# Kernel tuning notes

Measured on AMD Instinct MI355X. Metric: run time of the kernel, lower is better.

Reference implementation:

```python
import jax, jax.numpy as jnp
import numpy as np

N = 50000      # nodes
E = 400000     # edges per meta-path
DIN = 256      # input_dim
H = 4          # heads
F = 64         # output_dim per head
P = 3          # meta-paths
HID = 128      # SA_Attention hidden
NEG_SLOPE = 0.2


def setup_inputs() -> dict:
    key = jax.random.key(0)
    ks = jax.random.split(key, 12)
    inp = {
        "h": jax.random.normal(ks[0], (N, DIN), dtype=jnp.float32),
        "ei_0": jax.random.randint(ks[1], (2, E), 0, N, dtype=jnp.int64),
        "ei_1": jax.random.randint(ks[2], (2, E), 0, N, dtype=jnp.int64),
        "ei_2": jax.random.randint(ks[3], (2, E), 0, N, dtype=jnp.int64),
        # GAT params per meta-path (stacked over P)
        "gat_W": jax.random.normal(ks[4], (P, DIN, H * F), dtype=jnp.float32) * 0.05,
        "att_src": jax.random.normal(ks[5], (P, H, F), dtype=jnp.float32) * 0.05,
        "att_dst": jax.random.normal(ks[6], (P, H, F), dtype=jnp.float32) * 0.05,
        "gat_bias": jnp.zeros((P, H * F), dtype=jnp.float32),
        # SA_Attention params: Linear(H*F, HID) + Tanh + Linear(HID, 1, bias=False)
        "sa_w1": jax.random.normal(ks[7], (H * F, HID), dtype=jnp.float32) * 0.05,
        "sa_b1": jnp.zeros((HID,), dtype=jnp.float32),
        "sa_w2": jax.random.normal(ks[8], (HID,), dtype=jnp.float32) * 0.05,
    }
    return inp


def _gat_conv(x, ei, W, a_src, a_dst, b):
    """PyG-style GATConv with self-loops, concat heads. x:[N,DIN] -> [N,H*F]."""
    n = x.shape[0]
    xw = (x @ W).reshape(n, H, F)                    # [N,H,F]
    loop = jnp.arange(n, dtype=ei.dtype)
    src = jnp.concatenate([ei[0], loop])             # [E+N]
    dst = jnp.concatenate([ei[1], loop])
    alpha_s = jnp.einsum('nhf,hf->nh', xw, a_src)    # [N,H]
    alpha_d = jnp.einsum('nhf,hf->nh', xw, a_dst)
    e = jax.nn.leaky_relu(alpha_s[src] + alpha_d[dst], NEG_SLOPE)  # [E+N,H]
    # segment softmax over destination nodes (every node has a self loop)
    m = jax.ops.segment_max(e, dst, num_segments=n)
    ex = jnp.exp(e - m[dst])
    s = jax.ops.segment_sum(ex, dst, num_segments=n)
    alpha = ex / s[dst]                              # [E+N,H]
    out = jax.ops.segment_sum(alpha[:, :, None] * xw[src], dst, num_segments=n)
    return out.reshape(n, H * F) + b


def reference(h, ei_0, ei_1, ei_2, gat_W, att_src, att_dst, gat_bias,
              sa_w1, sa_b1, sa_w2):
    eis = [ei_0, ei_1, ei_2]
    # per-meta-path GAT embeddings -> z: [N, P, H*F]
    z = jnp.stack([
        _gat_conv(h, eis[i], gat_W[i], att_src[i], att_dst[i], gat_bias[i])
        for i in range(P)
    ], axis=1)
    # semantic attention: project -> mean over nodes -> softmax over meta-paths
    w = jnp.tanh(z @ sa_w1 + sa_b1) @ sa_w2          # [N,P]
    beta = jax.nn.softmax(w.mean(axis=0))            # [P]
    return (beta[None, :, None] * z).sum(axis=1)     # [N, H*F]
```

## Files before the change

### kernel.cpp

```cpp
#include <hip/hip_runtime.h>
#include <hip/hip_bf16.h>

__device__ __forceinline__ float bf2f(unsigned short u) {
    union { unsigned int i; float f; } x;
    x.i = ((unsigned int)u) << 16;
    return x.f;
}
__device__ __forceinline__ unsigned short f2bf(float f) {
    union { float f; unsigned int u; } x; x.f = f;
    unsigned int r = x.u + 0x7FFFu + ((x.u >> 16) & 1u);
    return (unsigned short)(r >> 16);
}
__device__ __forceinline__ float fast_tanh(float x) {
    float a = fabsf(x);
    float t = __expf(2.f * a);
    float r = 1.f - 2.f / (t + 1.f);
    return copysignf(r, x);
}

typedef __bf16    bf16x8 __attribute__((ext_vector_type(8)));
typedef _Float16  f16x8  __attribute__((ext_vector_type(8)));
typedef _Float16  f16x4  __attribute__((ext_vector_type(4)));
typedef float     f32x4  __attribute__((ext_vector_type(4)));
typedef unsigned short u16x8 __attribute__((ext_vector_type(8)));

#define XW_OFF     0UL
#define ZB_OFF     25600000UL
#define CSR_OFF    102400000UL
#define RS_OFF     107200000UL
#define CUR_OFF    107800064UL
#define BS_OFF     108400128UL
#define AS_OFF     108401152UL
#define AD_OFF     109201152UL
#define WT_OFF     110001152UL
#define W1T_OFF    110394368UL
#define ASF_OFF    110459904UL
#define ADF_OFF    110462976UL
#define BIASF_OFF  110466048UL
#define B1F_OFF    110469120UL
#define W2F_OFF    110469632UL
#define WSUM_OFF   110470144UL
#define BETA_OFF   110470208UL
#define FLAG_OFF   110470272UL

#define CHUNKA 5000
#define NBMAX  152
#define CAPB   16384

__global__ void probe(const unsigned short* __restrict__ hraw,
                      const unsigned int* __restrict__ eraw,
                      int* __restrict__ flags) {
    if (threadIdx.x == 0 && blockIdx.x == 0) {
        int sane = 0;
        for (int i = 0; i < 256; ++i) {
            unsigned int e = (hraw[i] >> 7) & 0xFF;
            if (hraw[i] != 0 && e >= 100 && e <= 150) sane++;
        }
        flags[0] = (sane >= 220) ? 1 : 0;
        int zeros = 0;
        for (int i = 1; i < 256; i += 2) if (eraw[i] == 0u) zeros++;
        flags[1] = (zeros >= 120) ? 1 : 0;
    }
}

__device__ __forceinline__ float rd_f(const void* p, int j, bool bf) {
    return bf ? bf2f(((const unsigned short*)p)[j]) : ((const float*)p)[j];
}
__device__ __forceinline__ int rd_i(const void* p, long long j, bool i64) {
    return i64 ? (int)((const long long*)p)[j] : ((const int*)p)[j];
}

__global__ void ingest_params(const void* W, const void* as, const void* ad, const void* bias,
                              const void* w1, const void* b1, const void* w2,
                              unsigned short* Wt, _Float16* w1t,
                              float* asf, float* adf, float* biasf,
                              float* b1f, float* w2f,
                              const int* __restrict__ flags) {
    int i = blockIdx.x * 256 + threadIdx.x;
    bool bf = flags[0] != 0;
    if (i < 196608) {
        int p = i >> 16, n = (i >> 8) & 255, k = i & 255;
        Wt[i] = f2bf(rd_f(W, p * 65536 + k * 256 + n, bf));
    } else if (i < 229376) {
        int j = i - 196608;
        int n = j >> 8, k = j & 255;
        w1t[j] = (_Float16)rd_f(w1, k * 128 + n, bf);
    } else if (i < 230144) {
        int j = i - 229376; asf[j] = rd_f(as, j, bf);
    } else if (i < 230912) {
        int j = i - 230144; adf[j] = rd_f(ad, j, bf);
    } else if (i < 231680) {
        int j = i - 230912; biasf[j] = rd_f(bias, j, bf);
    } else if (i < 231808) {
        int j = i - 231680; b1f[j] = rd_f(b1, j, bf);
    } else if (i < 231936) {
        int j = i - 231808; w2f[j] = rd_f(w2, j, bf);
    }
}

__global__ __launch_bounds__(256)
void bucket_a(const void* e0, const void* e1, const void* e2,
              int* __restrict__ bcnt, unsigned int* __restrict__ bkt,
              int E, int N, int NB, const int* __restrict__ flags) {
    __shared__ unsigned int  ent[CHUNKA];
    __shared__ unsigned char bck[CHUNKA];
    __shared__ unsigned int  sent[CHUNKA];
    __shared__ unsigned char sbck[CHUNKA];
    __shared__ int lcnt[NBMAX], lpre[NBMAX], lbase[NBMAX], lcur[NBMAX];
    int tid = threadIdx.x;
    int s = blockIdx.x * CHUNKA;
    int tot = 3 * E;
    int n = min(tot, s + CHUNKA) - s;
    for (int b = tid; b < NBMAX; b += 256) { lcnt[b] = 0; lcur[b] = 0; }
    __syncthreads();
    bool i64 = flags[1] != 0;
    for (int i = tid; i < n; i += 256) {
        int idx = s + i;
        int p = (idx >= 2 * E) ? 2 : (idx >= E) ? 1 : 0;
        int j = idx - p * E;
        const void* ep = (p == 0) ? e0 : (p == 1) ? e1 : e2;
        unsigned int src = (unsigned int)rd_i(ep, j, i64);
        unsigned int dst = (unsigned int)rd_i(ep, (long long)E + j, i64);
        int seg = p * N + (int)dst;
        int b = seg >> 10;
        ent[i] = src | ((unsigned int)(seg & 1023) << 16);
        bck[i] = (unsigned char)b;
        atomicAdd(&lcnt[b], 1);
    }
    __syncthreads();
    if (tid == 0) {
        int run = 0;
        for (int b = 0; b < NB; ++b) { lpre[b] = run; run += lcnt[b]; }
    }
    if (tid < NB) lbase[tid] = atomicAdd(&bcnt[tid], lcnt[tid]);
    __syncthreads();
    for (int i = tid; i < n; i += 256) {
        int b = bck[i];
        int pos = lpre[b] + atomicAdd(&lcur[b], 1);
        sent[pos] = ent[i];
        sbck[pos] = (unsigned char)b;
    }
    __syncthreads();
    for (int q = tid; q < n; q += 256) {
        int b = sbck[q];
        int gpos = lbase[b] + (q - lpre[b]);
        if (gpos < CAPB) bkt[(size_t)b * CAPB + gpos] = sent[q];
    }
}

__global__ __launch_bounds__(256)
void bucket_b(const int* __restrict__ bcnt, const unsigned int* __restrict__ bkt,
              int* __restrict__ rs, unsigned short* __restrict__ csr,
              int M, int NB, int tot) {
    __shared__ int scnt[1024];
    __shared__ int spre[1024];
    __shared__ int part[256];
    int b = blockIdx.x, tid = threadIdx.x;
    int acc = 0;
    for (int i = tid; i < b; i += 256) acc += min(bcnt[i], CAPB);
    part[tid] = acc; __syncthreads();
    for (int o = 128; o > 0; o >>= 1) {
        if (tid < o) part[tid] += part[tid + o];
        __syncthreads();
    }
    int base = part[0];
    int cnt = min(bcnt[b], CAPB);
    for (int i = tid; i < 1024; i += 256) scnt[i] = 0;
    __syncthreads();
    const unsigned int* src = bkt + (size_t)b * CAPB;
    for (int i = tid; i < cnt; i += 256)
        atomicAdd(&scnt[src[i] >> 16], 1);
    __syncthreads();
    int a0 = scnt[tid * 4], a1 = scnt[tid * 4 + 1], a2 = scnt[tid * 4 + 2], a3 = scnt[tid * 4 + 3];
    int psum = a0 + a1 + a2 + a3;
    part[tid] = psum; __syncthreads();
    for (int o = 1; o < 256; o <<= 1) {
        int tmp = (tid >= o) ? part[tid - o] : 0;
        __syncthreads();
        part[tid] += tmp;
        __syncthreads();
    }
    int pb = part[tid] - psum;
    spre[tid * 4]     = pb;
    spre[tid * 4 + 1] = pb + a0;
    spre[tid * 4 + 2] = pb + a0 + a1;
    spre[tid * 4 + 3] = pb + a0 + a1 + a2;
    __syncthreads();
    for (int i = tid; i < 1024; i += 256) {
        int seg = b * 1024 + i;
        if (seg < M) rs[seg] = base + spre[i];
        scnt[i] = 0;
    }
    if (b == NB - 1 && tid == 0) rs[M] = tot;
    __syncthreads();
    for (int i = tid; i < cnt; i += 256) {
        unsigned int u = src[i];
        int slow = u >> 16;
        int pos = spre[slow] + atomicAdd(&scnt[slow], 1);
        csr[base + pos] = (unsigned short)(u & 0xFFFFu);
    }
}

__global__ __launch_bounds__(1024, 4)
void gemm_xw_mfma(const void* __restrict__ h,
                  const unsigned short* __restrict__ Wtp,
                  unsigned short* __restrict__ xw,
                  const float* __restrict__ asf,
                  const float* __restrict__ adf,
                  float* __restrict__ as_, float* __restrict__ ad_,
                  const int* __restrict__ flags, int N) {
    __shared__ __bf16 Bs[32768];
    int tid  = threadIdx.x;
    int D = blockIdx.x;
    int qch = gridDim.x >> 3;
    int logical = (D & 7) * qch + (D >> 3);
    int ch   = logical & 1;
    int rg   = logical >> 1;
    {
        const bf16x8* src = (const bf16x8*)Wtp;
#pragma unroll
        for (int it = 0; it < 4; ++it) {
            int c = it * 1024 + tid;
            int row = c >> 5, cv = c & 31;
            *(bf16x8*)(Bs + ((row << 5) + (cv ^ (row & 7))) * 8) =
                src[(ch * 128 + row) * 32 + cv];
        }
    }
    __syncthreads();

    int wave = tid >> 6, lane = tid & 63;
    int l15 = lane & 15, quad = lane >> 4;
    int sw  = l15 & 7;
    int row0 = rg * 256 + wave * 16;
    bool bfm = flags[0] != 0;

    int lr = min(row0 + l15, N - 1);

    bf16x8 a[8];
    if (bfm) {
        const bf16x8* hp = reinterpret_cast<const bf16x8*>((const __bf16*)h + (size_t)lr * 256);
#pragma unroll
        for (int t = 0; t < 8; ++t) a[t] = hp[t * 4 + quad];
    } else {
        const float* hp = (const float*)h + (size_t)lr * 256;
#pragma unroll
        for (int t = 0; t < 8; ++t) {
            int off = t * 32 + quad * 8;
            f32x4 u0 = *reinterpret_cast<const f32x4*>(hp + off);
            f32x4 u1 = *reinterpret_cast<const f32x4*>(hp + off + 4);
#pragma unroll
            for (int j = 0; j < 4; ++j) { a[t][j] = (__bf16)u0[j]; a[t][4 + j] = (__bf16)u1[j]; }
        }
    }

    f32x4 acc[8];
#pragma unroll
    for (int tn = 0; tn < 8; ++tn) acc[tn] = (f32x4){0.f, 0.f, 0.f, 0.f};

#pragma unroll
    for (int t = 0; t < 8; ++t) {
        int c0 = t * 4;
#pragma unroll
        for (int tn = 0; tn < 8; ++tn) {
            int row = tn * 16 + l15;
            bf16x8 b = *reinterpret_cast<const bf16x8*>(
                Bs + ((row << 5) + ((c0 + quad) ^ sw)) * 8);
            acc[tn] = __builtin_amdgcn_mfma_f32_16x16x32_bf16(a[t], b, acc[tn], 0, 0, 0);
        }
    }

    int rbase = row0 + quad * 4;
#pragma unroll
    for (int tn = 0; tn < 8; ++tn) {
        int c = ch * 128 + tn * 16 + l15;
#pragma unroll
        for (int i = 0; i < 4; ++i) {
            int r = rbase + i;
            if (r < N) xw[(size_t)r * 256 + c] = f2bf(acc[tn][i]);
        }
    }
    float ss[2][4] = {{0.f,0.f,0.f,0.f},{0.f,0.f,0.f,0.f}};
    float dd[2][4] = {{0.f,0.f,0.f,0.f},{0.f,0.f,0.f,0.f}};
#pragma unroll
    for (int tn = 0; tn < 8; ++tn) {
        int c = ch * 128 + tn * 16 + l15;
        float sv = asf[c], dv = adf[c];
        int hs = tn >> 2;
#pragma unroll
        for (int i = 0; i < 4; ++i) {
            ss[hs][i] += acc[tn][i] * sv;
            dd[hs][i] += acc[tn][i] * dv;
        }
    }
#pragma unroll
    for (int hs = 0; hs < 2; ++hs)
#pragma unroll
        for (int i = 0; i < 4; ++i) {
            float s = ss[hs][i], d = dd[hs][i];
            s += __shfl_xor(s, 1); d += __shfl_xor(d, 1);
            s += __shfl_xor(s, 2); d += __shfl_xor(d, 2);
            s += __shfl_xor(s, 4); d += __shfl_xor(d, 4);
            s += __shfl_xor(s, 8); d += __shfl_xor(d, 8);
            ss[hs][i] = s; dd[hs][i] = d;
        }
    if (l15 == 0) {
#pragma unroll
        for (int hs = 0; hs < 2; ++hs)
#pragma unroll
            for (int i = 0; i < 4; ++i) {
                int r = rbase + i;
                if (r < N) {
                    int g = r * 4 + ch * 2 + hs;
                    as_[g] = ss[hs][i];
                    ad_[g] = dd[hs][i];
                }
            }
    }
}

__device__ __forceinline__ float leaky(float v) { return v > 0.f ? v : 0.2f * v; }

__global__ void agg_csr(const unsigned short* __restrict__ csr, const int* __restrict__ rs,
                        const float* __restrict__ as_, const float* __restrict__ ad_,
                        const unsigned short* __restrict__ xw,
                        const float* __restrict__ biasf,
                        _Float16* __restrict__ zb, int N, int p) {
    int d = blockIdx.x * 4 + (threadIdx.x >> 6);
    if (d >= N) return;
    int lane = threadIdx.x & 63;
    int half = lane >> 5;
    int l31  = lane & 31;
    int col8 = l31 * 8;
    int h    = col8 >> 6;
    int seg = p * N + d;
    int start = rs[seg], end = rs[seg + 1];

    float adh = ad_[d * 4 + h];
    float m = leaky(as_[d * 4 + h] + adh);
    float l = (half == 0) ? 1.f : 0.f;
    float a[8];
    {
        u16x8 u = *reinterpret_cast<const u16x8*>(xw + (size_t)d * 256 + col8);
#pragma unroll
        for (int k = 0; k < 8; ++k) a[k] = (half == 0) ? bf2f(u[k]) : 0.f;
    }

    if (start < end) {
        int i0 = min(start + half, end - 1);
        int srcA = csr[i0];
        float eA = (start + half < end) ? leaky(as_[srcA * 4 + h] + adh) : -1e30f;
        u16x8 xA = *reinterpret_cast<const u16x8*>(xw + (size_t)srcA * 256 + col8);
        for (int jb = start; jb < end; jb += 2) {
            int nidx = jb + 2 + half;
            int ni = min(nidx, end - 1);
            int srcB = csr[ni];
            float eB = (nidx < end) ? leaky(as_[srcB * 4 + h] + adh) : -1e30f;
            u16x8 xB = *reinterpret_cast<const u16x8*>(xw + (size_t)srcB * 256 + col8);
            float eO = __shfl_xor(eA, 32);
            float mn = fmaxf(m, fmaxf(eA, eO));
            float c  = __expf(m - mn);
            float w  = __expf(eA - mn);
            m = mn;
            l = l * c + w;
#pragma unroll
            for (int k = 0; k < 8; ++k)
                a[k] = a[k] * c + w * bf2f(xA[k]);
            srcA = srcB; eA = eB; xA = xB;
        }
    }
    l += __shfl_xor(l, 32);
#pragma unroll
    for (int k = 0; k < 8; ++k) a[k] += __shfl_xor(a[k], 32);

    if (half == 0) {
        float inv = 1.f / l;
        const float* bp = biasf + p * 256 + col8;
        f16x8 o;
#pragma unroll
        for (int k = 0; k < 8; ++k) o[k] = (_Float16)(a[k] * inv + bp[k]);
        *reinterpret_cast<f16x8*>(zb + ((size_t)d * 3 + p) * 256 + col8) = o;
    }
}

__global__ __launch_bounds__(1024, 4)
void sem_w_mfma(const _Float16* __restrict__ zb,
                const _Float16* __restrict__ w1t,
                const float* __restrict__ b1f,
                const float* __restrict__ w2f,
                float* __restrict__ wsum, int rows) {
    __shared__ _Float16 Bs[32768];
    __shared__ float redbuf[16][3];
    int tid = threadIdx.x;
    {
        const f16x8* src = (const f16x8*)w1t;
#pragma unroll
        for (int it = 0; it < 4; ++it) {
            int c = it * 1024 + tid;
            int row = c >> 5, cv = c & 31;
            *(f16x8*)(Bs + ((row << 5) + (cv ^ (row & 7))) * 8) = src[c];
        }
    }
    __syncthreads();

    int wave = tid >> 6, lane = tid & 63;
    int l15 = lane & 15, quad = lane >> 4;
    int sw  = l15 & 7;
    int row0 = blockIdx.x * 256 + wave * 16;
    int lr = min(row0 + l15, rows - 1);

    f16x8 a[8];
    {
        const f16x8* zp = reinterpret_cast<const f16x8*>(zb + (size_t)lr * 256);
#pragma unroll
        for (int t = 0; t < 8; ++t) a[t] = zp[t * 4 + quad];
    }

    f32x4 acc[8];
#pragma unroll
    for (int tn = 0; tn < 8; ++tn) acc[tn] = (f32x4){0.f, 0.f, 0.f, 0.f};

#pragma unroll
    for (int t = 0; t < 8; ++t) {
        int c0 = t * 4;
#pragma unroll
        for (int tn = 0; tn < 8; ++tn) {
            int brow = tn * 16 + l15;
            f16x8 b = *reinterpret_cast<const f16x8*>(
                Bs + ((brow << 5) + ((c0 + quad) ^ sw)) * 8);
            acc[tn] = __builtin_amdgcn_mfma_f32_16x16x32_f16(a[t], b, acc[tn], 0, 0, 0);
        }
    }

    float rowsum[4] = {0.f, 0.f, 0.f, 0.f};
#pragma unroll
    for (int tn = 0; tn < 8; ++tn) {
        int col = tn * 16 + l15;
        float b1v = b1f[col], w2v = w2f[col];
#pragma unroll
        for (int i = 0; i < 4; ++i)
            rowsum[i] += fast_tanh(acc[tn][i] + b1v) * w2v;
    }
#pragma unroll
    for (int i = 0; i < 4; ++i) {
        rowsum[i] += __shfl_xor(rowsum[i], 1);
        rowsum[i] += __shfl_xor(rowsum[i], 2);
        rowsum[i] += __shfl_xor(rowsum[i], 4);
        rowsum[i] += __shfl_xor(rowsum[i], 8);
    }
    float bins[3] = {0.f, 0.f, 0.f};
    if (l15 == 0) {
#pragma unroll
        for (int i = 0; i < 4; ++i) {
            int r = row0 + quad * 4 + i;
            if (r < rows) bins[r % 3] += rowsum[i];
        }
    }
#pragma unroll
    for (int b = 0; b < 3; ++b) {
        bins[b] += __shfl_xor(bins[b], 16);
        bins[b] += __shfl_xor(bins[b], 32);
    }
    if (lane == 0) {
#pragma unroll
        for (int b = 0; b < 3; ++b) redbuf[wave][b] = bins[b];
    }
    __syncthreads();
    if (tid < 3) {
        float s = 0.f;
#pragma unroll
        for (int w = 0; w < 16; ++w) s += redbuf[w][tid];
        atomicAdd(&wsum[tid], s);
    }
}

__global__ void combine(const _Float16* __restrict__ zb,
                        const float* __restrict__ wsum, float invN,
                        void* __restrict__ out, const int* __restrict__ flags) {
    int idx = blockIdx.x * 256 + threadIdx.x;
    int n = idx >> 6, c4 = (idx & 63) * 4;
    float w0 = wsum[0] * invN, w1 = wsum[1] * invN, w2 = wsum[2] * invN;
    float mx = fmaxf(w0, fmaxf(w1, w2));
    float e0 = __expf(w0 - mx), e1 = __expf(w1 - mx), e2 = __expf(w2 - mx);
    float s = 1.f / (e0 + e1 + e2);
    float b0 = e0 * s, b1 = e1 * s, b2 = e2 * s;
    const _Float16* base = zb + (size_t)n * 768 + c4;
    f16x4 z0 = *reinterpret_cast<const f16x4*>(base);
    f16x4 z1 = *reinterpret_cast<const f16x4*>(base + 256);
    f16x4 z2 = *reinterpret_cast<const f16x4*>(base + 512);
    float v[4];
#pragma unroll
    for (int i = 0; i < 4; ++i)
        v[i] = b0 * (float)z0[i] + b1 * (float)z1[i] + b2 * (float)z2[i];
    if (flags[0]) {
        ushort4 o = {f2bf(v[0]), f2bf(v[1]), f2bf(v[2]), f2bf(v[3])};
        *reinterpret_cast<ushort4*>((unsigned short*)out + (size_t)idx * 4) = o;
    } else {
        f32x4 o = {v[0], v[1], v[2], v[3]};
        *reinterpret_cast<f32x4*>((float*)out + (size_t)idx * 4) = o;
    }
}

extern "C" void kernel_launch(void* const* d_in, const int* in_sizes, int n_in,
                              void* d_out, int out_size, void* d_ws, size_t ws_size,
                              hipStream_t stream) {
    const void* h    = d_in[0];
    const void* e0   = d_in[1];
    const void* e1   = d_in[2];
    const void* e2   = d_in[3];
    const void* W    = d_in[4];
    const void* as   = d_in[5];
    const void* ad   = d_in[6];
    const void* bias = d_in[7];
    const void* w1   = d_in[8];
    const void* b1   = d_in[9];
    const void* w2   = d_in[10];

    const int N = in_sizes[0] / 256;
    const int E = in_sizes[1] / 2;
    const int M = 3 * N;
    const int NB = (M + 1023) >> 10;

    char* ws = (char*)d_ws;
    unsigned short* xw    = (unsigned short*)(ws + XW_OFF);
    _Float16*       zb    = (_Float16*)(ws + ZB_OFF);
    unsigned short* csr   = (unsigned short*)(ws + CSR_OFF);
    int*            rs    = (int*)(ws + RS_OFF);
    unsigned short* Wt    = (unsigned short*)(ws + WT_OFF);
    _Float16*       w1t   = (_Float16*)(ws + W1T_OFF);
    float*          asf   = (float*)(ws + ASF_OFF);
    float*          adf   = (float*)(ws + ADF_OFF);
    float*          biasf = (float*)(ws + BIASF_OFF);
    float*          b1f   = (float*)(ws + B1F_OFF);
    float*          w2f   = (float*)(ws + W2F_OFF);
    float*          wsum  = (float*)(ws + WSUM_OFF);
    float*          as_   = (float*)(ws + AS_OFF);
    float*          ad_   = (float*)(ws + AD_OFF);
    int*            flags = (int*)(ws + FLAG_OFF);

    unsigned int* bkt  = (unsigned int*)(ws + ZB_OFF);
    int*          bcnt = (int*)(ws + ZB_OFF + (size_t)NBMAX * CAPB * 4);

    probe<<<1, 64, 0, stream>>>((const unsigned short*)h, (const unsigned int*)e0, flags);
    ingest_params<<<907, 256, 0, stream>>>(W, as, ad, bias, w1, b1, w2,
                                           Wt, w1t, asf, adf, biasf, b1f, w2f, flags);

    hipMemsetAsync(bcnt, 0, NBMAX * sizeof(int), stream);
    int aBlocks = (3 * E + CHUNKA - 1) / CHUNKA;
    bucket_a<<<aBlocks, 256, 0, stream>>>(e0, e1, e2, bcnt, bkt, E, N, NB, flags);
    bucket_b<<<NB, 256, 0, stream>>>(bcnt, bkt, rs, csr, M, NB, 3 * E);

    hipMemsetAsync(wsum, 0, 16, stream);

    int gemmBlocks = ((N + 255) / 256) * 2;
    int aggBlocks  = (N + 3) / 4;
    for (int p = 0; p < 3; ++p) {
        gemm_xw_mfma<<<gemmBlocks, 1024, 0, stream>>>(h, Wt + p * 65536, xw,
                                                      asf + p * 256, adf + p * 256,
                                                      as_, ad_, flags, N);
        agg_csr<<<aggBlocks, 256, 0, stream>>>(csr, rs, as_, ad_, xw, biasf, zb, N, p);
    }

    int semBlocks = (M + 255) / 256;
    sem_w_mfma<<<semBlocks, 1024, 0, stream>>>(zb, w1t, b1f, w2f, wsum, M);
    combine<<<(N * 64 + 255) / 256, 256, 0, stream>>>(zb, wsum, 1.0f / (float)N, d_out, flags);
}
```

Measured before the change: 442.5 us.

## Fuse the three per-meta-path XW GEMMs into one launch reusing loaded h rows

The GEMM kernel now loops over all three meta-path weight matrices inside one launch. It loads each block's h row fragment into registers once and reloads only the weight tile into LDS per path. Separate xw and attention-score buffers are kept per path, and the workspace layout is recomputed so they fit, falling back to the old per-path launches if the workspace is too small. This cuts repeated reads of h and two launches, but costs about three times the xw buffer and gives up any overlap between GEMM and aggregation.

Result: no change. 449.0 us (+1.5%).

```diff
diff --git a/kernel.cpp b/kernel.cpp
--- a/kernel.cpp
+++ b/kernel.cpp
@@ -28,8 +28,6 @@
 #define ZB_OFF     25600000UL
 #define CSR_OFF    102400000UL
 #define RS_OFF     107200000UL
-#define CUR_OFF    107800064UL
-#define BS_OFF     108400128UL
 #define AS_OFF     108401152UL
 #define AD_OFF     109201152UL
 #define WT_OFF     110001152UL
@@ -40,7 +38,6 @@
 #define B1F_OFF    110469120UL
 #define W2F_OFF    110469632UL
 #define WSUM_OFF   110470144UL
-#define BETA_OFF   110470208UL
 #define FLAG_OFF   110470272UL
 
 #define CHUNKA 5000
@@ -203,12 +200,12 @@
 
 __global__ __launch_bounds__(1024, 4)
 void gemm_xw_mfma(const void* __restrict__ h,
-                  const unsigned short* __restrict__ Wtp,
+                  const unsigned short* __restrict__ Wt,
                   unsigned short* __restrict__ xw,
                   const float* __restrict__ asf,
                   const float* __restrict__ adf,
                   float* __restrict__ as_, float* __restrict__ ad_,
-                  const int* __restrict__ flags, int N) {
+                  const int* __restrict__ flags, int N, int pcount) {
     __shared__ __bf16 Bs[32768];
     int tid  = threadIdx.x;
     int D = blockIdx.x;
@@ -216,24 +213,12 @@
     int logical = (D & 7) * qch + (D >> 3);
     int ch   = logical & 1;
     int rg   = logical >> 1;
-    {
-        const bf16x8* src = (const bf16x8*)Wtp;
-#pragma unroll
-        for (int it = 0; it < 4; ++it) {
-            int c = it * 1024 + tid;
-            int row = c >> 5, cv = c & 31;
-            *(bf16x8*)(Bs + ((row << 5) + (cv ^ (row & 7))) * 8) =
-                src[(ch * 128 + row) * 32 + cv];
-        }
-    }
-    __syncthreads();
 
     int wave = tid >> 6, lane = tid & 63;
     int l15 = lane & 15, quad = lane >> 4;
     int sw  = l15 & 7;
     int row0 = rg * 256 + wave * 16;
     bool bfm = flags[0] != 0;
-
     int lr = min(row0 + l15, N - 1);
 
     bf16x8 a[8];
@@ -253,68 +238,88 @@
         }
     }
 
-    f32x4 acc[8];
-#pragma unroll
-    for (int tn = 0; tn < 8; ++tn) acc[tn] = (f32x4){0.f, 0.f, 0.f, 0.f};
-
-#pragma unroll
-    for (int t = 0; t < 8; ++t) {
-        int c0 = t * 4;
+    for (int p = 0; p < pcount; ++p) {
+        if (p) __syncthreads();
+        {
+            const bf16x8* src = (const bf16x8*)(Wt + (size_t)p * 65536);
+#pragma unroll
+            for (int it = 0; it < 4; ++it) {
+                int c = it * 1024 + tid;
+                int row = c >> 5, cv = c & 31;
+                *(bf16x8*)(Bs + ((row << 5) + (cv ^ (row & 7))) * 8) =
+                    src[(ch * 128 + row) * 32 + cv];
+            }
+        }
+        __syncthreads();
+
+        f32x4 acc[8];
+#pragma unroll
+        for (int tn = 0; tn < 8; ++tn) acc[tn] = (f32x4){0.f, 0.f, 0.f, 0.f};
+
+#pragma unroll
+        for (int t = 0; t < 8; ++t) {
+            int c0 = t * 4;
+#pragma unroll
+            for (int tn = 0; tn < 8; ++tn) {
+                int row = tn * 16 + l15;
+                bf16x8 b = *reinterpret_cast<const bf16x8*>(
+                    Bs + ((row << 5) + ((c0 + quad) ^ sw)) * 8);
+                acc[tn] = __builtin_amdgcn_mfma_f32_16x16x32_bf16(a[t], b, acc[tn], 0, 0, 0);
+            }
+        }
+
+        unsigned short* xwp = xw + (size_t)p * N * 256;
+        const float* asfp = asf + p * 256;
+        const float* adfp = adf + p * 256;
+        float* asp = as_ + (size_t)p * N * 4;
+        float* adp = ad_ + (size_t)p * N * 4;
+        int rbase = row0 + quad * 4;
 #pragma unroll
         for (int tn = 0; tn < 8; ++tn) {
-            int row = tn * 16 + l15;
-            bf16x8 b = *reinterpret_cast<const bf16x8*>(
-                Bs + ((row << 5) + ((c0 + quad) ^ sw)) * 8);
-            acc[tn] = __builtin_amdgcn_mfma_f32_16x16x32_bf16(a[t], b, acc[tn], 0, 0, 0);
-        }
-    }
-
-    int rbase = row0 + quad * 4;
-#pragma unroll
-    for (int tn = 0; tn < 8; ++tn) {
-        int c = ch * 128 + tn * 16 + l15;
-#pragma unroll
-        for (int i = 0; i < 4; ++i) {
-            int r = rbase + i;
-            if (r < N) xw[(size_t)r * 256 + c] = f2bf(acc[tn][i]);
-        }
-    }
-    float ss[2][4] = {{0.f,0.f,0.f,0.f},{0.f,0.f,0.f,0.f}};
-    float dd[2][4] = {{0.f,0.f,0.f,0.f},{0.f,0.f,0.f,0.f}};
-#pragma unroll
-    for (int tn = 0; tn < 8; ++tn) {
-        int c = ch * 128 + tn * 16 + l15;
-        float sv = asf[c], dv = adf[c];
-        int hs = tn >> 2;
-#pragma unroll
-        for (int i = 0; i < 4; ++i) {
-            ss[hs][i] += acc[tn][i] * sv;
-            dd[hs][i] += acc[tn][i] * dv;
-        }
-    }
-#pragma unroll
-    for (int hs = 0; hs < 2; ++hs)
-#pragma unroll
-        for (int i = 0; i < 4; ++i) {
-            float s = ss[hs][i], d = dd[hs][i];
-            s += __shfl_xor(s, 1); d += __shfl_xor(d, 1);
-            s += __shfl_xor(s, 2); d += __shfl_xor(d, 2);
-            s += __shfl_xor(s, 4); d += __shfl_xor(d, 4);
-            s += __shfl_xor(s, 8); d += __shfl_xor(d, 8);
-            ss[hs][i] = s; dd[hs][i] = d;
-        }
-    if (l15 == 0) {
-#pragma unroll
-        for (int hs = 0; hs < 2; ++hs)
+            int c = ch * 128 + tn * 16 + l15;
 #pragma unroll
             for (int i = 0; i < 4; ++i) {
                 int r = rbase + i;
-                if (r < N) {
-                    int g = r * 4 + ch * 2 + hs;
-                    as_[g] = ss[hs][i];
-                    ad_[g] = dd[hs][i];
+                if (r < N) xwp[(size_t)r * 256 + c] = f2bf(acc[tn][i]);
+            }
+        }
+        float ss[2][4] = {{0.f,0.f,0.f,0.f},{0.f,0.f,0.f,0.f}};
+        float dd[2][4] = {{0.f,0.f,0.f,0.f},{0.f,0.f,0.f,0.f}};
+#pragma unroll
+        for (int tn = 0; tn < 8; ++tn) {
+            int c = ch * 128 + tn * 16 + l15;
+            float sv = asfp[c], dv = adfp[c];
+            int hs = tn >> 2;
+#pragma unroll
+            for (int i = 0; i < 4; ++i) {
+                ss[hs][i] += acc[tn][i] * sv;
+                dd[hs][i] += acc[tn][i] * dv;
+            }
+        }
+#pragma unroll
+        for (int hs = 0; hs < 2; ++hs)
+#pragma unroll
+            for (int i = 0; i < 4; ++i) {
+                float s = ss[hs][i], d = dd[hs][i];
+                s += __shfl_xor(s, 1); d += __shfl_xor(d, 1);
+                s += __shfl_xor(s, 2); d += __shfl_xor(d, 2);
+                s += __shfl_xor(s, 4); d += __shfl_xor(d, 4);
+                s += __shfl_xor(s, 8); d += __shfl_xor(d, 8);
+                ss[hs][i] = s; dd[hs][i] = d;
+            }
+        if (l15 == 0) {
+#pragma unroll
+            for (int hs = 0; hs < 2; ++hs)
+#pragma unroll
+                for (int i = 0; i < 4; ++i) {
+                    int r = rbase + i;
+                    if (r < N) {
+                        int g = r * 4 + ch * 2 + hs;
+                        asp[g] = ss[hs][i];
+                        adp[g] = dd[hs][i];
+                    }
                 }
-            }
+        }
     }
 }
 
@@ -521,24 +526,66 @@
     const int NB = (M + 1023) >> 10;
 
     char* ws = (char*)d_ws;
-    unsigned short* xw    = (unsigned short*)(ws + XW_OFF);
-    _Float16*       zb    = (_Float16*)(ws + ZB_OFF);
-    unsigned short* csr   = (unsigned short*)(ws + CSR_OFF);
-    int*            rs    = (int*)(ws + RS_OFF);
-    unsigned short* Wt    = (unsigned short*)(ws + WT_OFF);
-    _Float16*       w1t   = (_Float16*)(ws + W1T_OFF);
-    float*          asf   = (float*)(ws + ASF_OFF);
-    float*          adf   = (float*)(ws + ADF_OFF);
-    float*          biasf = (float*)(ws + BIASF_OFF);
-    float*          b1f   = (float*)(ws + B1F_OFF);
-    float*          w2f   = (float*)(ws + W2F_OFF);
-    float*          wsum  = (float*)(ws + WSUM_OFF);
-    float*          as_   = (float*)(ws + AS_OFF);
-    float*          ad_   = (float*)(ws + AD_OFF);
-    int*            flags = (int*)(ws + FLAG_OFF);
-
-    unsigned int* bkt  = (unsigned int*)(ws + ZB_OFF);
-    int*          bcnt = (int*)(ws + ZB_OFF + (size_t)NBMAX * CAPB * 4);
+
+    auto al = [](size_t x) { return (x + 255) & ~(size_t)255; };
+    size_t o = 0;
+    size_t oXW3 = o; o += al((size_t)3 * N * 256 * 2);
+    size_t oZB  = o; o += al((size_t)3 * N * 256 * 2);
+    size_t oCSR = o; o += al((size_t)3 * E * 2);
+    size_t oRS  = o; o += al((size_t)(3 * N + 1) * 4);
+    size_t oAS3 = o; o += al((size_t)3 * N * 4 * 4);
+    size_t oAD3 = o; o += al((size_t)3 * N * 4 * 4);
+    size_t oWT  = o; o += al(196608UL * 2);
+    size_t oW1T = o; o += al(32768UL * 2);
+    size_t oASF = o; o += al(768 * 4);
+    size_t oADF = o; o += al(768 * 4);
+    size_t oBIA = o; o += al(768 * 4);
+    size_t oB1  = o; o += al(128 * 4);
+    size_t oW2  = o; o += al(128 * 4);
+    size_t oWSU = o; o += al(64);
+    size_t oFLG = o; o += al(64);
+    bool fused = (ws_size >= o);
+
+    unsigned short *xw, *csr, *Wt;
+    _Float16 *zb, *w1t;
+    int *rs, *flags;
+    float *asf, *adf, *biasf, *b1f, *w2f, *wsum, *as_, *ad_;
+    if (fused) {
+        xw    = (unsigned short*)(ws + oXW3);
+        zb    = (_Float16*)(ws + oZB);
+        csr   = (unsigned short*)(ws + oCSR);
+        rs    = (int*)(ws + oRS);
+        as_   = (float*)(ws + oAS3);
+        ad_   = (float*)(ws + oAD3);
+        Wt    = (unsigned short*)(ws + oWT);
+        w1t   = (_Float16*)(ws + oW1T);
+        asf   = (float*)(ws + oASF);
+        adf   = (float*)(ws + oADF);
+        biasf = (float*)(ws + oBIA);
+        b1f   = (float*)(ws + oB1);
+        w2f   = (float*)(ws + oW2);
+        wsum  = (float*)(ws + oWSU);
+        flags = (int*)(ws + oFLG);
+    } else {
+        xw    = (unsigned short*)(ws + XW_OFF);
+        zb    = (_Float16*)(ws + ZB_OFF);
+        csr   = (unsigned short*)(ws + CSR_OFF);
+        rs    = (int*)(ws + RS_OFF);
+        as_   = (float*)(ws + AS_OFF);
+        ad_   = (float*)(ws + AD_OFF);
+        Wt    = (unsigned short*)(ws + WT_OFF);
+        w1t   = (_Float16*)(ws + W1T_OFF);
+        asf   = (float*)(ws + ASF_OFF);
+        adf   = (float*)(ws + ADF_OFF);
+        biasf = (float*)(ws + BIASF_OFF);
+        b1f   = (float*)(ws + B1F_OFF);
+        w2f   = (float*)(ws + W2F_OFF);
+        wsum  = (float*)(ws + WSUM_OFF);
+        flags = (int*)(ws + FLAG_OFF);
+    }
+
+    unsigned int* bkt  = (unsigned int*)zb;
+    int*          bcnt = (int*)((char*)zb + (size_t)NBMAX * CAPB * 4);
 
     probe<<<1, 64, 0, stream>>>((const unsigned short*)h, (const unsigned int*)e0, flags);
     ingest_params<<<907, 256, 0, stream>>>(W, as, ad, bias, w1, b1, w2,
@@ -553,11 +600,22 @@
 
     int gemmBlocks = ((N + 255) / 256) * 2;
     int aggBlocks  = (N + 3) / 4;
-    for (int p = 0; p < 3; ++p) {
-        gemm_xw_mfma<<<gemmBlocks, 1024, 0, stream>>>(h, Wt + p * 65536, xw,
-                                                      asf + p * 256, adf + p * 256,
-                                                      as_, ad_, flags, N);
-        agg_csr<<<aggBlocks, 256, 0, stream>>>(csr, rs, as_, ad_, xw, biasf, zb, N, p);
+    if (fused) {
+        gemm_xw_mfma<<<gemmBlocks, 1024, 0, stream>>>(h, Wt, xw, asf, adf,
+                                                      as_, ad_, flags, N, 3);
+        for (int p = 0; p < 3; ++p)
+            agg_csr<<<aggBlocks, 256, 0, stream>>>(csr, rs,
+                                                   as_ + (size_t)p * N * 4,
+                                                   ad_ + (size_t)p * N * 4,
+                                                   xw + (size_t)p * N * 256,
+                                                   biasf, zb, N, p);
+    } else {
+        for (int p = 0; p < 3; ++p) {
+            gemm_xw_mfma<<<gemmBlocks, 1024, 0, stream>>>(h, Wt + (size_t)p * 65536, xw,
+                                                          asf + p * 256, adf + p * 256,
+                                                          as_, ad_, flags, N, 1);
+            agg_csr<<<aggBlocks, 256, 0, stream>>>(csr, rs, as_, ad_, xw, biasf, zb, N, p);
+        }
     }
 
     int semBlocks = (M + 255) / 256;
```
